# Performance work log

Hardware: AMD Instinct MI355X
Metric: run time of the kernel (lower is better)

## Reference

```python
import jax, jax.numpy as jnp
import numpy as np

TAU = 0.1
N_HEADS = 8


def rosa_scan(x):
    """Per-diagonal recurrence y[r,c] = x[r,c] * (y[r-1,c-1] + 1) on the lower
    triangle of each [T,T] matrix; upper triangle of the output is 0.
    Implemented by skewing diagonals into the scan axis and using an
    associative scan with combine (g,a)*(g',a') = (g'*g, g'*a + a').
    x: [N, T, T] float."""
    N, T, _ = x.shape
    n = jnp.arange(T)
    # Skew: S[b, pos, d] = x[b, pos + d, pos] (element #pos of diagonal d)
    rows = n[:, None] + n[None, :]          # [pos, d]
    valid = rows < T
    rows_c = jnp.where(valid, rows, 0)
    cols = jnp.broadcast_to(n[:, None], (T, T))
    S = x[:, rows_c, cols]                  # [N, T(pos), T(d)]
    g = jnp.where(valid[None], S, 1.0)      # identity element (1, 0) as padding
    a = jnp.where(valid[None], S, 0.0)

    def comb(c1, c2):
        g0, a0 = c1
        g1, a1 = c2
        return (g1 * g0, g1 * a0 + a1)

    _, A = jax.lax.associative_scan(comb, (g, a), axis=1)
    # Unskew: y[b, r, c] = A[b, pos=c, d=r-c] for r>=c else 0
    d = n[:, None] - n[None, :]             # [row, col]
    low = d >= 0
    dc = jnp.where(low, d, 0)
    colmat = jnp.broadcast_to(n[None, :], (T, T))
    return jnp.where(low[None], A[:, colmat, dc], 0.0)


def rosa_attn_score(x, tau):
    """x: [B, H, T, T] soft run-length scores -> causal softmax scores."""
    T = x.shape[-1]
    r = jnp.arange(T, dtype=x.dtype)
    p = r[None, :] / (r[:, None] + 1.0)     # position tiebreaker bias
    x = x + p
    mask = jnp.arange(T)[:, None] < jnp.arange(T)[None, :]  # upper triangle
    x = jnp.where(mask, -jnp.inf, x)
    return jax.nn.softmax(x / tau, axis=-1)


def setup_inputs() -> dict:
    key = jax.random.key(0)
    ks = jax.random.split(key, 5)
    B, T, D, Hd = 2, 1024, 512, 64
    x = jax.random.normal(ks[0], (B, T, D), dtype=jnp.float32)
    wq = jax.random.normal(ks[1], (D, D), dtype=jnp.float32) * 0.05
    wk = jax.random.normal(ks[2], (D, D), dtype=jnp.float32) * 0.05
    wv = jax.random.normal(ks[3], (D, D), dtype=jnp.float32) * 0.05
    wo = jax.random.normal(ks[4], (D, Hd), dtype=jnp.float32) * 0.05
    return {"x": x, "wq": wq, "wk": wk, "wv": wv, "wo": wo}


def reference(x, wq, wk, wv, wo):
    B, T, D = x.shape
    H = N_HEADS
    Hd = D // H
    tau = TAU
    iq = jax.nn.softmax((x @ wq).reshape(B, T, H, Hd) / tau, axis=-1)
    ik = jax.nn.softmax((x @ wk).reshape(B, T, H, Hd) / tau, axis=-1)
    iv = jax.nn.softmax((x @ wv).reshape(B, T, H, Hd) / tau, axis=-1)
    # a[b,h,t,s] = iq[b,t,h,:] . ik[b,s,h,:]
    a = jnp.einsum("bthd,bshd->bhts", iq, ik)
    a = rosa_scan(a.reshape(B * H, T, T)).reshape(B, H, T, T)
    a = rosa_attn_score(a, tau)
    o = jnp.einsum("bhts,bshd->bhtd", a, iv)
    xv = wo.reshape(H, Hd, Hd)
    o = jnp.einsum("bhtd,hde->bhte", o, xv)
    return o.transpose(0, 2, 1, 3).reshape(B, T, D)
```

## Files before the change

kernel.cpp:

```cpp
#include <hip/hip_runtime.h>
#include <hip/hip_bf16.h>
#include <math.h>


#define TT 1024
#define BB 2
#define HH 8
#define HD 64
#define DD 512
#define BH (BB*HH)

constexpr float INV_TAU = 10.0f;

#define SW(r, j) ((j) ^ ((((r) >> 2) & 7) << 2))

__global__ __launch_bounds__(256) void k_proj(const float* __restrict__ x,
                                              const float* __restrict__ wq,
                                              const float* __restrict__ wk,
                                              const float* __restrict__ wv,
                                              float* __restrict__ oq,
                                              float* __restrict__ ok,
                                              float* __restrict__ ov) {
  __shared__ float xs[16][512];
  const int tid = threadIdx.x;
  const int arr = blockIdx.y;
  const float* __restrict__ W = (arr == 0) ? wq : ((arr == 1) ? wk : wv);
  float* __restrict__ out = (arr == 0) ? oq : ((arr == 1) ? ok : ov);
  const int row0 = blockIdx.x * 16;

  for (int idx = tid; idx < 16 * 512; idx += 256) {
    int r = idx >> 9, c = idx & 511;
    xs[r][c] = x[(size_t)(row0 + r) * 512 + c];
  }
  __syncthreads();

  float acc0[16] = {};
  float acc1[16] = {};
  for (int k = 0; k < 512; k += 4) {
    float wa[4], wb[4];
#pragma unroll
    for (int jj = 0; jj < 4; ++jj) {
      wa[jj] = W[(size_t)(k + jj) * 512 + tid];
      wb[jj] = W[(size_t)(k + jj) * 512 + 256 + tid];
    }
#pragma unroll
    for (int r = 0; r < 16; ++r) {
      float4 xv = *(const float4*)&xs[r][k];
      acc0[r] = fmaf(xv.x, wa[0], acc0[r]);
      acc0[r] = fmaf(xv.y, wa[1], acc0[r]);
      acc0[r] = fmaf(xv.z, wa[2], acc0[r]);
      acc0[r] = fmaf(xv.w, wa[3], acc0[r]);
      acc1[r] = fmaf(xv.x, wb[0], acc1[r]);
      acc1[r] = fmaf(xv.y, wb[1], acc1[r]);
      acc1[r] = fmaf(xv.z, wb[2], acc1[r]);
      acc1[r] = fmaf(xv.w, wb[3], acc1[r]);
    }
  }
#pragma unroll
  for (int r = 0; r < 16; ++r) {
    float m0 = acc0[r], m1 = acc1[r];
#pragma unroll
    for (int off = 32; off; off >>= 1) {
      m0 = fmaxf(m0, __shfl_xor(m0, off));
      m1 = fmaxf(m1, __shfl_xor(m1, off));
    }
    float e0 = __expf((acc0[r] - m0) * INV_TAU);
    float e1 = __expf((acc1[r] - m1) * INV_TAU);
    float s0 = e0, s1 = e1;
#pragma unroll
    for (int off = 32; off; off >>= 1) {
      s0 += __shfl_xor(s0, off);
      s1 += __shfl_xor(s1, off);
    }
    out[(size_t)(row0 + r) * 512 + tid]       = e0 / s0;
    out[(size_t)(row0 + r) * 512 + 256 + tid] = e1 / s1;
  }
}

__global__ __launch_bounds__(256) void k_qkt(const float* __restrict__ q,
                                             const float* __restrict__ k,
                                             float* __restrict__ S) {
  int bh = blockIdx.x / 136;
  int tri = blockIdx.x - bh * 136;
  int di = 0;
  while (tri >= 16 - di) { tri -= 16 - di; ++di; }
  int cj = tri;
  int d0 = di * 64, c0 = cj * 64;
  int b = bh >> 3, h = bh & 7;

  __shared__ float ks[64][64];
  __shared__ float qs[128][64];
  int tid = threadIdx.x;

  for (int idx = tid; idx < 64 * 64; idx += 256) {
    int r = idx >> 6, j = idx & 63;
    ks[r][SW(r, j)] = k[((size_t)(b * TT + c0 + r) * HH + h) * 64 + j];
  }
  int tb = c0 + d0;
  for (int idx = tid; idx < 128 * 64; idx += 256) {
    int r = idx >> 6, j = idx & 63;
    int t = tb + r;
    qs[r][SW(r, j)] = (t < TT) ? q[((size_t)(b * TT + t) * HH + h) * 64 + j] : 0.0f;
  }
  __syncthreads();

  int tx = tid & 15, ty = tid >> 4;
  int cl = tx * 4, dl = ty * 4;
  int qbase = cl + dl;
  float acc[4][4] = {};
  for (int j = 0; j < 64; j += 4) {
    float kv[4][4], qv[7][4];
#pragma unroll
    for (int i = 0; i < 4; ++i) {
      float4 t4 = *(const float4*)&ks[cl + i][SW(cl + i, j)];
      kv[i][0] = t4.x; kv[i][1] = t4.y; kv[i][2] = t4.z; kv[i][3] = t4.w;
    }
#pragma unroll
    for (int i = 0; i < 7; ++i) {
      float4 t4 = *(const float4*)&qs[qbase + i][SW(qbase + i, j)];
      qv[i][0] = t4.x; qv[i][1] = t4.y; qv[i][2] = t4.z; qv[i][3] = t4.w;
    }
#pragma unroll
    for (int jj = 0; jj < 4; ++jj)
#pragma unroll
      for (int m = 0; m < 4; ++m)
#pragma unroll
        for (int i = 0; i < 4; ++i)
          acc[m][i] = fmaf(qv[m + i][jj], kv[i][jj], acc[m][i]);
  }

  float* Sb = S + (size_t)bh * TT * TT;
#pragma unroll
  for (int m = 0; m < 4; ++m) {
    int d = d0 + dl + m;
#pragma unroll
    for (int i = 0; i < 4; ++i) {
      int c = c0 + cl + i;
      if (d + c < TT) Sb[(size_t)d * TT + c] = acc[m][i];
    }
  }
}

__global__ __launch_bounds__(256) void k_scan(float* __restrict__ S) {
  int gw = (blockIdx.x * 256 + threadIdx.x) >> 6;
  int lane = threadIdx.x & 63;
  int bh = gw >> 10;
  int d = gw & 1023;
  float* row = S + (size_t)bh * TT * TT + (size_t)d * TT;
  int len = TT - d;
  float carry = 0.0f;
  for (int c0 = 0; c0 < len; c0 += 64) {
    int c = c0 + lane;
    bool act = (c < len);
    float xv = act ? row[c] : 0.0f;
    float G = xv, A = xv;
#pragma unroll
    for (int off = 1; off < 64; off <<= 1) {
      float gp = __shfl_up(G, off);
      float ap = __shfl_up(A, off);
      if (lane >= off) { A = fmaf(G, ap, A); G *= gp; }
    }
    float y = fmaf(G, carry, A);
    if (act) row[c] = y;
    carry = __shfl(y, 63);
  }
}

__global__ __launch_bounds__(256) void k_attn_part(const float* __restrict__ S,
                                                   const float* __restrict__ v,
                                                   float* __restrict__ opart,
                                                   float* __restrict__ mpart,
                                                   float* __restrict__ lpart) {
  int bh = blockIdx.x / 272;
  int u = blockIdx.x - bh * 272;
  int tt = 0;
  while (true) { int nch = (tt + 2) >> 1; if (u < nch) break; u -= nch; ++tt; }
  int ci = u;
  int t0 = tt * 32, s0 = ci * 64;
  int b = bh >> 3, h = bh & 7;

  __shared__ float As[32][64];
  __shared__ float vs[64][64];
  int tid = threadIdx.x;
  int wv = tid >> 6, lane = tid & 63;

  for (int idx = tid; idx < 64 * 16; idx += 256) {
    int sl = idx >> 4, e4 = (idx & 15) << 2;
    *(float4*)&vs[sl][e4] =
        *(const float4*)&v[((size_t)(b * TT + s0 + sl) * HH + h) * 64 + e4];
  }
  const float* Sb = S + (size_t)bh * TT * TT;
  int dbase = t0 - s0 - 63;
  for (int idx = tid; idx < 95 * 64; idx += 256) {
    int dd = idx >> 6, sl = idx & 63;
    int d = dbase + dd;
    if (d < 0) continue;
    int tl = d + sl + s0 - t0;
    if (tl < 0 || tl >= 32) continue;
    As[tl][sl] = Sb[(size_t)d * TT + s0 + sl];
  }
  __syncthreads();

  int tlb = wv * 8;
  for (int r = 0; r < 8; ++r) {
    int tl = tlb + r;
    int t = t0 + tl;
    float inv_t1 = 1.0f / (float)(t + 1);
    bool okl = (s0 + lane <= t);
    float sc = okl ? As[tl][lane] + (float)(s0 + lane) * inv_t1 : -1e30f;
    float mt = sc;
#pragma unroll
    for (int off = 32; off; off >>= 1) mt = fmaxf(mt, __shfl_xor(mt, off));
    float p = __expf((sc - mt) * INV_TAU);
    float lsum = p;
#pragma unroll
    for (int off = 32; off; off >>= 1) lsum += __shfl_xor(lsum, off);
    As[tl][lane] = p;
    if (lane == 0) {
      size_t pidx = (size_t)(bh * TT + t) * 16 + ci;
      mpart[pidx] = mt; lpart[pidx] = lsum;
    }
  }
  float o[8] = {};
  for (int sl = 0; sl < 64; sl += 4) {
    float v0 = vs[sl + 0][lane];
    float v1 = vs[sl + 1][lane];
    float v2 = vs[sl + 2][lane];
    float v3 = vs[sl + 3][lane];
#pragma unroll
    for (int r = 0; r < 8; ++r) {
      float4 pq = *(const float4*)&As[tlb + r][sl];
      o[r] = fmaf(pq.x, v0, o[r]);
      o[r] = fmaf(pq.y, v1, o[r]);
      o[r] = fmaf(pq.z, v2, o[r]);
      o[r] = fmaf(pq.w, v3, o[r]);
    }
  }
#pragma unroll
  for (int r = 0; r < 8; ++r) {
    int t = t0 + tlb + r;
    opart[((size_t)(bh * TT + t) * 16 + ci) * 64 + lane] = o[r];
  }
}

__global__ __launch_bounds__(256) void k_combine(const float* __restrict__ opart,
                                                 const float* __restrict__ mpart,
                                                 const float* __restrict__ lpart,
                                                 const float* __restrict__ wo,
                                                 float* __restrict__ out) {
  int bh = blockIdx.x >> 8;
  int tg = blockIdx.x & 255;
  int b = bh >> 3, h = bh & 7;
  int tid = threadIdx.x;
  int wv = tid >> 6, lane = tid & 63;

  __shared__ float wos[64][64];
  for (int idx = tid; idx < 4096; idx += 256)
    (&wos[0][0])[idx] = wo[(size_t)h * 4096 + idx];
  __syncthreads();

  int t = tg * 4 + wv;
  int nc = (t >> 6) + 1;
  size_t base = (size_t)(bh * TT + t) * 16;

  float m = (lane < nc) ? mpart[base + lane] : -3e30f;
  float M = m;
#pragma unroll
  for (int off = 32; off; off >>= 1) M = fmaxf(M, __shfl_xor(M, off));
  float w = (lane < nc) ? __expf((m - M) * INV_TAU) : 0.0f;
  float lv = (lane < nc) ? lpart[base + lane] : 0.0f;
  float Lp = lv * w;
#pragma unroll
  for (int off = 32; off; off >>= 1) Lp += __shfl_xor(Lp, off);

  float o = 0.0f;
  for (int i = 0; i < nc; ++i) {
    float wi = __shfl(w, i);
    o = fmaf(wi, opart[(base + i) * 64 + lane], o);
  }
  float on = o / Lp;

  float res = 0.0f;
#pragma unroll 8
  for (int e = 0; e < 64; ++e)
    res = fmaf(__shfl(on, e), wos[e][lane], res);
  out[((size_t)(b * TT + t)) * 512 + h * 64 + lane] = res;
}

extern "C" void kernel_launch(void* const* d_in, const int* in_sizes, int n_in,
                              void* d_out, int out_size, void* d_ws, size_t ws_size,
                              hipStream_t stream) {
  const float* x  = (const float*)d_in[0];
  const float* wq = (const float*)d_in[1];
  const float* wk = (const float*)d_in[2];
  const float* wv = (const float*)d_in[3];
  const float* wo = (const float*)d_in[4];
  float* out = (float*)d_out;

  char* ws = (char*)d_ws;
  const size_t MB = 1024 * 1024;
  float* q     = (float*)(ws);
  float* k     = (float*)(ws + 4 * MB);
  float* v     = (float*)(ws + 8 * MB);
  float* S     = (float*)(ws + 12 * MB);
  float* opart = (float*)(ws + 76 * MB);
  float* mpart = (float*)(ws + 140 * MB);
  float* lpart = (float*)(ws + 141 * MB);

  k_proj<<<dim3(128, 3), 256, 0, stream>>>(x, wq, wk, wv, q, k, v);
  k_qkt<<<BH * 136, 256, 0, stream>>>(q, k, S);
  k_scan<<<4096, 256, 0, stream>>>(S);
  k_attn_part<<<BH * 272, 256, 0, stream>>>(S, v, opart, mpart, lpart);
  k_combine<<<4096, 256, 0, stream>>>(opart, mpart, lpart, wo, out);
}
```

Before: 328.9 us.

## Rework projection kernel: 8-row tiles, float2 columns, drop shared-memory staging

The QKV projection kernel now processes 8 rows per block instead of 16, doubling the grid. Each thread owns two adjacent output columns loaded as float2, and x is read straight from global memory rather than staged in shared memory. The head softmax reduction now spans 32 lanes with two values per lane. This aims to raise occupancy and parallelism for a small kernel, at the cost of more repeated global reads of x and W per output.

```diff
diff --git a/kernel.cpp b/kernel.cpp
--- a/kernel.cpp
+++ b/kernel.cpp
@@ -21,59 +21,45 @@
                                               float* __restrict__ oq,
                                               float* __restrict__ ok,
                                               float* __restrict__ ov) {
-  __shared__ float xs[16][512];
   const int tid = threadIdx.x;
   const int arr = blockIdx.y;
   const float* __restrict__ W = (arr == 0) ? wq : ((arr == 1) ? wk : wv);
   float* __restrict__ out = (arr == 0) ? oq : ((arr == 1) ? ok : ov);
-  const int row0 = blockIdx.x * 16;
-
-  for (int idx = tid; idx < 16 * 512; idx += 256) {
-    int r = idx >> 9, c = idx & 511;
-    xs[r][c] = x[(size_t)(row0 + r) * 512 + c];
-  }
-  __syncthreads();
-
-  float acc0[16] = {};
-  float acc1[16] = {};
+  const int row0 = blockIdx.x * 8;
+  const int c2 = tid * 2;
+
+  float a0[8] = {};
+  float a1[8] = {};
   for (int k = 0; k < 512; k += 4) {
-    float wa[4], wb[4];
-#pragma unroll
-    for (int jj = 0; jj < 4; ++jj) {
-      wa[jj] = W[(size_t)(k + jj) * 512 + tid];
-      wb[jj] = W[(size_t)(k + jj) * 512 + 256 + tid];
-    }
-#pragma unroll
-    for (int r = 0; r < 16; ++r) {
-      float4 xv = *(const float4*)&xs[r][k];
-      acc0[r] = fmaf(xv.x, wa[0], acc0[r]);
-      acc0[r] = fmaf(xv.y, wa[1], acc0[r]);
-      acc0[r] = fmaf(xv.z, wa[2], acc0[r]);
-      acc0[r] = fmaf(xv.w, wa[3], acc0[r]);
-      acc1[r] = fmaf(xv.x, wb[0], acc1[r]);
-      acc1[r] = fmaf(xv.y, wb[1], acc1[r]);
-      acc1[r] = fmaf(xv.z, wb[2], acc1[r]);
-      acc1[r] = fmaf(xv.w, wb[3], acc1[r]);
-    }
-  }
-#pragma unroll
-  for (int r = 0; r < 16; ++r) {
-    float m0 = acc0[r], m1 = acc1[r];
-#pragma unroll
-    for (int off = 32; off; off >>= 1) {
-      m0 = fmaxf(m0, __shfl_xor(m0, off));
-      m1 = fmaxf(m1, __shfl_xor(m1, off));
-    }
-    float e0 = __expf((acc0[r] - m0) * INV_TAU);
-    float e1 = __expf((acc1[r] - m1) * INV_TAU);
-    float s0 = e0, s1 = e1;
-#pragma unroll
-    for (int off = 32; off; off >>= 1) {
-      s0 += __shfl_xor(s0, off);
-      s1 += __shfl_xor(s1, off);
-    }
-    out[(size_t)(row0 + r) * 512 + tid]       = e0 / s0;
-    out[(size_t)(row0 + r) * 512 + 256 + tid] = e1 / s1;
+    float2 w01[4];
+#pragma unroll
+    for (int jj = 0; jj < 4; ++jj)
+      w01[jj] = *(const float2*)&W[(size_t)(k + jj) * 512 + c2];
+#pragma unroll
+    for (int r = 0; r < 8; ++r) {
+      float4 xv = *(const float4*)&x[(size_t)(row0 + r) * 512 + k];
+      a0[r] = fmaf(xv.x, w01[0].x, a0[r]);
+      a1[r] = fmaf(xv.x, w01[0].y, a1[r]);
+      a0[r] = fmaf(xv.y, w01[1].x, a0[r]);
+      a1[r] = fmaf(xv.y, w01[1].y, a1[r]);
+      a0[r] = fmaf(xv.z, w01[2].x, a0[r]);
+      a1[r] = fmaf(xv.z, w01[2].y, a1[r]);
+      a0[r] = fmaf(xv.w, w01[3].x, a0[r]);
+      a1[r] = fmaf(xv.w, w01[3].y, a1[r]);
+    }
+  }
+#pragma unroll
+  for (int r = 0; r < 8; ++r) {
+    float m01 = fmaxf(a0[r], a1[r]);
+#pragma unroll
+    for (int off = 16; off; off >>= 1) m01 = fmaxf(m01, __shfl_xor(m01, off));
+    float e0 = __expf((a0[r] - m01) * INV_TAU);
+    float e1 = __expf((a1[r] - m01) * INV_TAU);
+    float s = e0 + e1;
+#pragma unroll
+    for (int off = 16; off; off >>= 1) s += __shfl_xor(s, off);
+    float inv = 1.0f / s;
+    *(float2*)&out[(size_t)(row0 + r) * 512 + c2] = make_float2(e0 * inv, e1 * inv);
   }
 }
 
@@ -307,7 +293,7 @@
   float* mpart = (float*)(ws + 140 * MB);
   float* lpart = (float*)(ws + 141 * MB);
 
-  k_proj<<<dim3(128, 3), 256, 0, stream>>>(x, wq, wk, wv, q, k, v);
+  k_proj<<<dim3(256, 3), 256, 0, stream>>>(x, wq, wk, wv, q, k, v);
   k_qkt<<<BH * 136, 256, 0, stream>>>(q, k, S);
   k_scan<<<4096, 256, 0, stream>>>(S);
   k_attn_part<<<BH * 272, 256, 0, stream>>>(S, v, opart, mpart, lpart);
```

Result: faster. 319.6 us (-2.8%).
